# Performance work log

Hardware: AMD Instinct MI355X
Metric: run time of the kernel (lower is better)

## Reference

```python
import math
import jax, jax.numpy as jnp
import numpy as np

HEADS = 2
HEAD_NUMS = 4
BS, C, NR, NC = 16, 256, 96, 96


def _sa(x, mask, kw, kb, qw, qb, vw, vb):
    # x: [B, C, N] (Conv1d k=1 == per-position linear), mask: [B, N] floats in {0,1}
    B, Cc, N = x.shape
    H = HEAD_NUMS
    D = Cc // H
    scale = 1.0 / math.sqrt(D)

    def proj(w, b):
        return (jnp.einsum('dc,bcn->bdn', w, x) + b[None, :, None]).reshape(B, H, D, N)

    k = proj(kw, kb)
    q = proj(qw, qb)
    v = proj(vw, vb)
    # logits[b,h,n,m] = sum_d k[b,h,d,n] * q[b,h,d,m]; softmax over m, mask on m
    logits = jnp.einsum('bhdn,bhdm->bhnm', k, q) * scale
    mbool = mask > 0
    logits = jnp.where(mbool[:, None, None, :], logits, jnp.asarray(-1e30, x.dtype))
    w = jax.nn.softmax(logits, axis=-1)
    out = jnp.einsum('bhdm,bhnm->bhdn', v, w).reshape(B, Cc, N)
    # fully-masked sequences (padded grid rows/cols) -> zero instead of NaN
    valid = jnp.any(mbool, axis=-1)  # [B]
    out = jnp.where(valid[:, None, None], out, jnp.zeros((), x.dtype))
    return out + x


def setup_inputs() -> dict:
    key = jax.random.key(0)
    ks = jax.random.split(key, 16)
    num_rows = jax.random.randint(ks[0], (BS,), NR // 2, NR + 1, dtype=jnp.int32)
    num_cols = jax.random.randint(ks[1], (BS,), NC // 2, NC + 1, dtype=jnp.int32)
    feats = jax.random.normal(ks[2], (BS, C, NR, NC), dtype=jnp.float32)
    # aligned cell features are zero in padded region (align_cells_feat pads with 0)
    rmask = (jnp.arange(NR)[None, :] < num_rows[:, None])
    cmask = (jnp.arange(NC)[None, :] < num_cols[:, None])
    grid = (rmask[:, :, None] & cmask[:, None, :]).astype(jnp.float32)
    feats = feats * grid[:, None, :, :]
    inp = {'feats': feats, 'num_rows': num_rows, 'num_cols': num_cols}
    names = ['col_k', 'col_q', 'col_v', 'row_k', 'row_q', 'row_v']
    for i, nm in enumerate(names):
        inp[nm + '_w'] = 0.02 * jax.random.normal(ks[3 + 2 * i], (HEADS, C, C), dtype=jnp.float32)
        inp[nm + '_b'] = 0.02 * jax.random.normal(ks[4 + 2 * i], (HEADS, C), dtype=jnp.float32)
    return inp


def reference(feats, num_rows, num_cols,
              col_k_w, col_k_b, col_q_w, col_q_b, col_v_w, col_v_b,
              row_k_w, row_k_b, row_q_w, row_q_b, row_v_w, row_v_b):
    bs, c, nr, nc = feats.shape
    rmask = (jnp.arange(nr)[None, :] < num_rows[:, None])
    cmask = (jnp.arange(nc)[None, :] < num_cols[:, None])
    masks = (rmask[:, :, None] & cmask[:, None, :]).astype(feats.dtype)  # [bs, nr, nc]
    x = feats
    for i in range(HEADS):
        # column attention: sequences along nc, one per (batch, row)
        xc = x.transpose(0, 2, 1, 3).reshape(bs * nr, c, nc)
        mc = masks.reshape(bs * nr, nc)
        xc = _sa(xc, mc, col_k_w[i], col_k_b[i], col_q_w[i], col_q_b[i], col_v_w[i], col_v_b[i])
        x = xc.reshape(bs, nr, c, nc).transpose(0, 2, 1, 3)
        # row attention: sequences along nr, one per (batch, col)
        xr = x.transpose(0, 3, 1, 2).reshape(bs * nc, c, nr)
        mr = masks.transpose(0, 2, 1).reshape(bs * nc, nr)
        xr = _sa(xr, mr, row_k_w[i], row_k_b[i], row_q_w[i], row_q_b[i], row_v_w[i], row_v_b[i])
        x = xr.reshape(bs, nc, c, nr).transpose(0, 2, 3, 1)
    return x, masks
```

## Files before the change

kernel.cpp:

```cpp
#include <hip/hip_runtime.h>

typedef __attribute__((ext_vector_type(8))) short bf16x8;
typedef __attribute__((ext_vector_type(4))) float f32x4;

#define MFMA16(a, b, c) __builtin_amdgcn_mfma_f32_16x16x32_bf16(a, b, c, 0, 0, 0)

__device__ __forceinline__ unsigned short f2bf(float f) {
    unsigned int u = __float_as_uint(f);
    u += 0x7FFFu + ((u >> 16) & 1u);
    return (unsigned short)(u >> 16);
}
__device__ __forceinline__ float bf2f(unsigned short h) {
    return __uint_as_float(((unsigned int)h) << 16);
}

struct WPtrs { const float* p[6]; };

__global__ __launch_bounds__(256) void conv_w_kernel(WPtrs wp, unsigned short* dst) {
    int idx = blockIdx.x * 256 + threadIdx.x;
    if (idx >= 196608) return;
    int t = idx >> 15;
    int q = idx & 32767;
    float4 v = *(const float4*)(wp.p[t] + ((size_t)q << 2));
    ushort4 o;
    o.x = f2bf(v.x); o.y = f2bf(v.y); o.z = f2bf(v.z); o.w = f2bf(v.w);
    *(ushort4*)(dst + ((size_t)t << 17) + ((size_t)q << 2)) = o;
}

__global__ __launch_bounds__(256) void t_in(const float* __restrict__ feats,
                                            unsigned short* __restrict__ dst) {
    __shared__ unsigned short t[96 * 257];
    const int b = blockIdx.x / 96, r = blockIdx.x % 96;
    const int tid = threadIdx.x;
    for (int i = tid; i < 6144; i += 256) {
        const int c = i / 24, q4 = i % 24;
        float4 v = *(const float4*)(feats + ((size_t)(b * 256 + c) * 9216) + r * 96 + q4 * 4);
        t[(q4 * 4 + 0) * 257 + c] = f2bf(v.x);
        t[(q4 * 4 + 1) * 257 + c] = f2bf(v.y);
        t[(q4 * 4 + 2) * 257 + c] = f2bf(v.z);
        t[(q4 * 4 + 3) * 257 + c] = f2bf(v.w);
    }
    __syncthreads();
    for (int i = tid; i < 3072; i += 256) {
        const int q = i / 32, co = i % 32;
        unsigned short ob[8];
#pragma unroll
        for (int j = 0; j < 8; ++j) ob[j] = t[q * 257 + co * 8 + j];
        *(uint4*)(dst + ((size_t)(b * 96 + r) * 96 + q) * 256 + co * 8) = *(const uint4*)ob;
    }
}

__global__ __launch_bounds__(256) void final_k(const unsigned short* __restrict__ x,
                                               float* __restrict__ out) {
    __shared__ unsigned short t[256 * 97];
    const int b = blockIdx.x / 96, r = blockIdx.x % 96;
    const int tid = threadIdx.x;
    const unsigned short* sg = x + (size_t)(b * 96 + r) * 24576;
    for (int i = tid; i < 3072; i += 256) {
        const int q = i / 32, co = i % 32;
        uint4 v = *(const uint4*)(sg + (size_t)q * 256 + co * 8);
        const unsigned short* pv = (const unsigned short*)&v;
#pragma unroll
        for (int j = 0; j < 8; ++j) t[(co * 8 + j) * 97 + q] = pv[j];
    }
    __syncthreads();
    for (int i = tid; i < 6144; i += 256) {
        const int c = i / 24, q4 = i % 24;
        float4 f;
        f.x = bf2f(t[c * 97 + q4 * 4 + 0]);
        f.y = bf2f(t[c * 97 + q4 * 4 + 1]);
        f.z = bf2f(t[c * 97 + q4 * 4 + 2]);
        f.w = bf2f(t[c * 97 + q4 * 4 + 3]);
        *(float4*)(out + ((size_t)(b * 256 + c) * 9216) + r * 96 + q4 * 4) = f;
    }
}

__global__ __launch_bounds__(256) void masks_kernel(const int* __restrict__ nr,
                                                    const int* __restrict__ nc,
                                                    float* __restrict__ out) {
    int i = blockIdx.x * 256 + threadIdx.x;
    if (i >= 147456) return;
    int b = i / 9216, rem = i % 9216, r = rem / 96, c = rem % 96;
    out[i] = (r < nr[b] && c < nc[b]) ? 1.0f : 0.0f;
}

#define KT_S 72
#define VM_S 104
#define PM_S 104
#define OT_S 101

__global__ __launch_bounds__(384, 4) void sa3(
    const unsigned short* __restrict__ src, unsigned short* __restrict__ dst,
    const unsigned short* __restrict__ Wk, const unsigned short* __restrict__ Wq,
    const unsigned short* __restrict__ Wv,
    const float* __restrict__ bk, const float* __restrict__ bq, const float* __restrict__ bv,
    const int* __restrict__ lim_s, const int* __restrict__ lim_m) {
    extern __shared__ char smem[];
    unsigned short* Kt = (unsigned short*)smem;
    unsigned short* Qt = (unsigned short*)(smem + 13824);
    unsigned short* Vm = (unsigned short*)(smem + 27648);
    unsigned short* Pm = (unsigned short*)smem;
    float*          OT = (float*)smem;

    const int bid = blockIdx.x;
    const int grp = bid >> 5, l5 = bid & 31;
    const int h = l5 >> 3;
    const int seq = grp * 8 + (l5 & 7);
    const int b = seq / 96, s = seq % 96;
    const int tid = threadIdx.x;

    const unsigned short* sg = src + (size_t)seq * 24576;

    if (s >= lim_s[b]) {
        for (int i = tid; i < 768; i += 384) {
            const int n = i >> 3, c8 = i & 7;
            uint4 v = *(const uint4*)(sg + (size_t)n * 256 + h * 64 + c8 * 8);
            *(uint4*)(dst + ((size_t)(b * 96 + n) * 96 + s) * 256 + h * 64 + c8 * 8) = v;
        }
        return;
    }
    const int mlim = lim_m[b];

    const int wave = tid >> 6, lane = tid & 63, lr = lane & 15, lk = lane >> 4;
    const int p = wave >> 1, g = wave & 1;
    const unsigned short* Wp = (p == 0) ? Wk : (p == 1) ? Wq : Wv;
    const float* bp = (p == 0) ? bk : (p == 1) ? bq : bv;

    f32x4 acc[2][6];
#pragma unroll
    for (int dt = 0; dt < 2; ++dt)
#pragma unroll
        for (int nt = 0; nt < 6; ++nt) acc[dt][nt] = (f32x4)0.0f;

    const unsigned short* xb = sg + lr * 256 + lk * 8;
    const unsigned short* wb = Wp + (size_t)(h * 64 + g * 32 + lr) * 256 + lk * 8;
#pragma unroll
    for (int cc = 0; cc < 8; ++cc) {
        bf16x8 bfr[6];
#pragma unroll
        for (int nt = 0; nt < 6; ++nt)
            bfr[nt] = *(const bf16x8*)(xb + nt * 4096 + cc * 32);
#pragma unroll
        for (int dt = 0; dt < 2; ++dt) {
            bf16x8 afr = *(const bf16x8*)(wb + dt * 4096 + cc * 32);
#pragma unroll
            for (int nt = 0; nt < 6; ++nt)
                acc[dt][nt] = MFMA16(afr, bfr[nt], acc[dt][nt]);
        }
    }

    __syncthreads();

#pragma unroll
    for (int dt = 0; dt < 2; ++dt) {
        const int dbase = g * 32 + dt * 16 + lk * 4;
        const float b0 = bp[h * 64 + dbase + 0], b1 = bp[h * 64 + dbase + 1];
        const float b2 = bp[h * 64 + dbase + 2], b3 = bp[h * 64 + dbase + 3];
#pragma unroll
        for (int nt = 0; nt < 6; ++nt) {
            const int n = nt * 16 + lr;
            if (p == 2) {
                Vm[(dbase + 0) * VM_S + n] = f2bf(acc[dt][nt][0] + b0);
                Vm[(dbase + 1) * VM_S + n] = f2bf(acc[dt][nt][1] + b1);
                Vm[(dbase + 2) * VM_S + n] = f2bf(acc[dt][nt][2] + b2);
                Vm[(dbase + 3) * VM_S + n] = f2bf(acc[dt][nt][3] + b3);
            } else {
                ushort4 o;
                o.x = f2bf(acc[dt][nt][0] + b0);
                o.y = f2bf(acc[dt][nt][1] + b1);
                o.z = f2bf(acc[dt][nt][2] + b2);
                o.w = f2bf(acc[dt][nt][3] + b3);
                *(ushort4*)&((p == 0 ? Kt : Qt)[n * KT_S + dbase]) = o;
            }
        }
    }
    __syncthreads();

    f32x4 acc2[6];
#pragma unroll
    for (int mt = 0; mt < 6; ++mt) acc2[mt] = (f32x4)0.0f;
#pragma unroll
    for (int k0 = 0; k0 < 64; k0 += 32) {
        bf16x8 kf = *(const bf16x8*)&Kt[(wave * 16 + lr) * KT_S + k0 + lk * 8];
#pragma unroll
        for (int mt = 0; mt < 6; ++mt) {
            bf16x8 qf = *(const bf16x8*)&Qt[(mt * 16 + lr) * KT_S + k0 + lk * 8];
            acc2[mt] = MFMA16(kf, qf, acc2[mt]);
        }
    }
    __syncthreads();

    float lg[6][4];
#pragma unroll
    for (int mt = 0; mt < 6; ++mt) {
        const bool valid = (mt * 16 + lr) < mlim;
#pragma unroll
        for (int r2 = 0; r2 < 4; ++r2)
            lg[mt][r2] = valid ? acc2[mt][r2] * 0.125f : -3.0e38f;
    }
#pragma unroll
    for (int r2 = 0; r2 < 4; ++r2) {
        float mx = lg[0][r2];
#pragma unroll
        for (int mt = 1; mt < 6; ++mt) mx = fmaxf(mx, lg[mt][r2]);
        mx = fmaxf(mx, __shfl_xor(mx, 1));
        mx = fmaxf(mx, __shfl_xor(mx, 2));
        mx = fmaxf(mx, __shfl_xor(mx, 4));
        mx = fmaxf(mx, __shfl_xor(mx, 8));
        float sm = 0.0f;
#pragma unroll
        for (int mt = 0; mt < 6; ++mt) {
            float e = __expf(lg[mt][r2] - mx);
            lg[mt][r2] = e;
            sm += e;
        }
        sm += __shfl_xor(sm, 1);
        sm += __shfl_xor(sm, 2);
        sm += __shfl_xor(sm, 4);
        sm += __shfl_xor(sm, 8);
        const float inv = 1.0f / sm;
        const int n = wave * 16 + lk * 4 + r2;
#pragma unroll
        for (int mt = 0; mt < 6; ++mt)
            Pm[n * PM_S + mt * 16 + lr] = f2bf(lg[mt][r2] * inv);
    }
    __syncthreads();

    f32x4 acc3[4];
#pragma unroll
    for (int dt = 0; dt < 4; ++dt) acc3[dt] = (f32x4)0.0f;
    const int nk = (mlim + 31) >> 5;
    for (int k0i = 0; k0i < nk; ++k0i) {
        const int k0 = k0i * 32;
        bf16x8 pf = *(const bf16x8*)&Pm[(wave * 16 + lr) * PM_S + k0 + lk * 8];
#pragma unroll
        for (int dt = 0; dt < 4; ++dt) {
            bf16x8 vf = *(const bf16x8*)&Vm[(dt * 16 + lr) * VM_S + k0 + lk * 8];
            acc3[dt] = MFMA16(vf, pf, acc3[dt]);
        }
    }
    __syncthreads();

#pragma unroll
    for (int dt = 0; dt < 4; ++dt)
#pragma unroll
        for (int r2 = 0; r2 < 4; ++r2)
            OT[(dt * 16 + lk * 4 + r2) * OT_S + wave * 16 + lr] = acc3[dt][r2];
    __syncthreads();

    for (int i = tid; i < 768; i += 384) {
        const int n = i >> 3, c8 = i & 7;
        uint4 rv = *(const uint4*)(sg + (size_t)n * 256 + h * 64 + c8 * 8);
        const unsigned short* rs = (const unsigned short*)&rv;
        unsigned short ob[8];
#pragma unroll
        for (int j = 0; j < 8; ++j)
            ob[j] = f2bf(OT[(c8 * 8 + j) * OT_S + n] + bf2f(rs[j]));
        *(uint4*)(dst + ((size_t)(b * 96 + n) * 96 + s) * 256 + h * 64 + c8 * 8) = *(const uint4*)ob;
    }
}

extern "C" void kernel_launch(void* const* d_in, const int* in_sizes, int n_in,
                              void* d_out, int out_size, void* d_ws, size_t ws_size,
                              hipStream_t stream) {
    const float* feats    = (const float*)d_in[0];
    const int*   num_rows = (const int*)d_in[1];
    const int*   num_cols = (const int*)d_in[2];

    unsigned short* bufA = (unsigned short*)d_ws;
    unsigned short* wbuf = (unsigned short*)((char*)d_ws + 75497472);
    unsigned short* bufB = (unsigned short*)d_out;

    WPtrs wp;
    for (int t = 0; t < 6; ++t) wp.p[t] = (const float*)d_in[3 + 2 * t];

    (void)hipFuncSetAttribute((const void*)sa3,
                              hipFuncAttributeMaxDynamicSharedMemorySize, 40960);

    conv_w_kernel<<<768, 256, 0, stream>>>(wp, wbuf);
    t_in<<<1536, 256, 0, stream>>>(feats, bufA);

    unsigned short* cur = bufA;
    unsigned short* nxt = bufB;
    for (int i = 0; i < 2; ++i) {
        for (int dir = 0; dir < 2; ++dir) {
            const int tb = dir * 3;
            const unsigned short* Wk = wbuf + (size_t)(tb + 0) * 131072 + (size_t)i * 65536;
            const unsigned short* Wq = wbuf + (size_t)(tb + 1) * 131072 + (size_t)i * 65536;
            const unsigned short* Wv = wbuf + (size_t)(tb + 2) * 131072 + (size_t)i * 65536;
            const float* bk = (const float*)d_in[4 + 2 * (tb + 0)] + i * 256;
            const float* bq = (const float*)d_in[4 + 2 * (tb + 1)] + i * 256;
            const float* bv = (const float*)d_in[4 + 2 * (tb + 2)] + i * 256;
            const int* lim_s = (dir == 0) ? num_rows : num_cols;
            const int* lim_m = (dir == 0) ? num_cols : num_rows;
            sa3<<<6144, 384, 40960, stream>>>(cur, nxt, Wk, Wq, Wv, bk, bq, bv, lim_s, lim_m);
            unsigned short* t = cur; cur = nxt; nxt = t;
        }
    }

    final_k<<<1536, 256, 0, stream>>>(cur, (float*)d_out);
    masks_kernel<<<576, 256, 0, stream>>>(num_rows, num_cols, (float*)d_out + 37748736);
}
```

Before: 1.386 ms.

## Stage X tiles into LDS via async global_load_lds with double buffering

The projection GEMM now streams the shared input tile into LDS using direct global-to-LDS loads. It double-buffers over the channel chunks so each tile is fetched once per block instead of once per wave. The launch-bounds hint is raised and dynamic LDS grows to hold the staging buffers. The cost is a __syncthreads per chunk and a larger LDS footprint, which may cap occupancy below the new hint.

```diff
diff --git a/kernel.cpp b/kernel.cpp
--- a/kernel.cpp
+++ b/kernel.cpp
@@ -12,6 +12,12 @@
 }
 __device__ __forceinline__ float bf2f(unsigned short h) {
     return __uint_as_float(((unsigned int)h) << 16);
+}
+
+__device__ __forceinline__ void gload_lds16(const unsigned short* g, unsigned short* l) {
+    __builtin_amdgcn_global_load_lds(
+        (const __attribute__((address_space(1))) unsigned int*)(const void*)g,
+        (__attribute__((address_space(3))) unsigned int*)(void*)l, 16, 0, 0);
 }
 
 struct WPtrs { const float* p[6]; };
@@ -89,16 +95,17 @@
 #define PM_S 104
 #define OT_S 101
 
-__global__ __launch_bounds__(384, 4) void sa3(
+__global__ __launch_bounds__(384, 8) void sa4(
     const unsigned short* __restrict__ src, unsigned short* __restrict__ dst,
     const unsigned short* __restrict__ Wk, const unsigned short* __restrict__ Wq,
     const unsigned short* __restrict__ Wv,
     const float* __restrict__ bk, const float* __restrict__ bq, const float* __restrict__ bv,
     const int* __restrict__ lim_s, const int* __restrict__ lim_m) {
     extern __shared__ char smem[];
-    unsigned short* Kt = (unsigned short*)smem;
-    unsigned short* Qt = (unsigned short*)(smem + 13824);
-    unsigned short* Vm = (unsigned short*)(smem + 27648);
+    unsigned short* xs = (unsigned short*)smem;
+    unsigned short* Kt = (unsigned short*)(smem + 12288);
+    unsigned short* Qt = (unsigned short*)(smem + 26112);
+    unsigned short* Vm = (unsigned short*)(smem + 39936);
     unsigned short* Pm = (unsigned short*)smem;
     float*          OT = (float*)smem;
 
@@ -126,30 +133,36 @@
     const unsigned short* Wp = (p == 0) ? Wk : (p == 1) ? Wq : Wv;
     const float* bp = (p == 0) ? bk : (p == 1) ? bq : bv;
 
+    const int srow = wave * 16 + (lane >> 2);
+    const unsigned short* gstage = sg + srow * 256 + (lane & 3) * 8;
+    unsigned short* lstage = xs + wave * 512;
+    const unsigned short* wb = Wp + (size_t)(h * 64 + g * 32 + lr) * 256 + lk * 8;
+
     f32x4 acc[2][6];
 #pragma unroll
     for (int dt = 0; dt < 2; ++dt)
 #pragma unroll
         for (int nt = 0; nt < 6; ++nt) acc[dt][nt] = (f32x4)0.0f;
 
-    const unsigned short* xb = sg + lr * 256 + lk * 8;
-    const unsigned short* wb = Wp + (size_t)(h * 64 + g * 32 + lr) * 256 + lk * 8;
-#pragma unroll
+    gload_lds16(gstage, lstage);
+    __syncthreads();
+
+    int buf = 0;
     for (int cc = 0; cc < 8; ++cc) {
-        bf16x8 bfr[6];
-#pragma unroll
-        for (int nt = 0; nt < 6; ++nt)
-            bfr[nt] = *(const bf16x8*)(xb + nt * 4096 + cc * 32);
-#pragma unroll
-        for (int dt = 0; dt < 2; ++dt) {
-            bf16x8 afr = *(const bf16x8*)(wb + dt * 4096 + cc * 32);
-#pragma unroll
-            for (int nt = 0; nt < 6; ++nt)
-                acc[dt][nt] = MFMA16(afr, bfr[nt], acc[dt][nt]);
-        }
-    }
-
-    __syncthreads();
+        if (cc < 7)
+            gload_lds16(gstage + (cc + 1) * 32, lstage + (buf ^ 1) * 3072);
+        bf16x8 afr0 = *(const bf16x8*)(wb + cc * 32);
+        bf16x8 afr1 = *(const bf16x8*)(wb + 4096 + cc * 32);
+        const unsigned short* xc = xs + buf * 3072;
+#pragma unroll
+        for (int nt = 0; nt < 6; ++nt) {
+            bf16x8 bfr = *(const bf16x8*)&xc[(nt * 16 + lr) * 32 + lk * 8];
+            acc[0][nt] = MFMA16(afr0, bfr, acc[0][nt]);
+            acc[1][nt] = MFMA16(afr1, bfr, acc[1][nt]);
+        }
+        __syncthreads();
+        buf ^= 1;
+    }
 
 #pragma unroll
     for (int dt = 0; dt < 2; ++dt) {
@@ -274,8 +287,8 @@
     WPtrs wp;
     for (int t = 0; t < 6; ++t) wp.p[t] = (const float*)d_in[3 + 2 * t];
 
-    (void)hipFuncSetAttribute((const void*)sa3,
-                              hipFuncAttributeMaxDynamicSharedMemorySize, 40960);
+    (void)hipFuncSetAttribute((const void*)sa4,
+                              hipFuncAttributeMaxDynamicSharedMemorySize, 53248);
 
     conv_w_kernel<<<768, 256, 0, stream>>>(wp, wbuf);
     t_in<<<1536, 256, 0, stream>>>(feats, bufA);
@@ -293,7 +306,7 @@
             const float* bv = (const float*)d_in[4 + 2 * (tb + 2)] + i * 256;
             const int* lim_s = (dir == 0) ? num_rows : num_cols;
             const int* lim_m = (dir == 0) ? num_cols : num_rows;
-            sa3<<<6144, 384, 40960, stream>>>(cur, nxt, Wk, Wq, Wv, bk, bq, bv, lim_s, lim_m);
+            sa4<<<6144, 384, 53248, stream>>>(cur, nxt, Wk, Wq, Wv, bk, bq, bv, lim_s, lim_m);
             unsigned short* t = cur; cur = nxt; nxt = t;
         }
     }
```

New measurement: 1.431 ms. +3.2%, slower.
